# Optimization experiments

Hardware: AMD Instinct MI355X
Metric: run time of the kernel (lower is better)

Reference implementation:

```python
import jax, jax.numpy as jnp
import numpy as np

B, N, D = 32, 20, 64          # graph pairs, max node set size, node state dim
NODE_F, EDGE_F = 16, 8        # raw feature dims
E_PER, PROP = 40, 5           # edges per graph, propagation steps
NC2 = N * (N - 1) // 2        # 190
TEMP, ITERS = 0.1, 20         # sinkhorn temperature / iterations
SRC, DST = np.triu_indices(N, 1)   # source_list / destination_list (len NC2)


def _lin(k, fin, fout):
    return jax.random.normal(k, (fin, fout), dtype=jnp.float32) / np.sqrt(fin).astype(np.float32)


def setup_inputs():
    key = jax.random.key(0)
    ks = jax.random.split(key, 24)
    tn, te = 2 * B * N, 2 * B * E_PER
    gid = jnp.repeat(jnp.arange(2 * B), E_PER)   # edges stay within their graph
    inp = {
        'node_features': jax.random.normal(ks[0], (tn, NODE_F), jnp.float32),
        'edge_features': jax.random.normal(ks[1], (te, EDGE_F), jnp.float32),
        'query_adj': (jax.random.uniform(ks[2], (B, N, N)) < 0.3).astype(jnp.float32),
        'corpus_adj': (jax.random.uniform(ks[3], (B, N, N)) < 0.3).astype(jnp.float32),
        'from_idx': jax.random.randint(ks[4], (te,), 0, N) + gid * N,
        'to_idx': jax.random.randint(ks[5], (te,), 0, N) + gid * N,
    }
    # GraphEncoder
    inp['Wn'] = _lin(ks[6], NODE_F, D); inp['bn'] = jnp.zeros(D)
    inp['We'] = _lin(ks[7], EDGE_F, D); inp['be'] = jnp.zeros(D)
    # GraphPropLayer: message net (in 3D) and node-update net (in 2D)
    inp['Wm1'] = _lin(ks[8], 3 * D, D); inp['bm1'] = jnp.zeros(D)
    inp['Wm2'] = _lin(ks[9], D, D);     inp['bm2'] = jnp.zeros(D)
    inp['Wu1'] = _lin(ks[10], 2 * D, D); inp['bu1'] = jnp.zeros(D)
    inp['Wu2'] = _lin(ks[11], D, D);     inp['bu2'] = jnp.zeros(D)
    # node_sinkhorn_feature_layers: Linear(D,N) -> ReLU -> Linear(N,N)
    inp['Ws1'] = _lin(ks[12], D, N); inp['bs1'] = jnp.zeros(N)
    inp['Ws2'] = _lin(ks[13], N, N); inp['bs2'] = jnp.zeros(N)
    # lrl_network: Linear(2D+1, D) -> ReLU -> Linear(D, D)
    inp['Wl1'] = _lin(ks[14], 2 * D + 1, D); inp['bl1'] = jnp.zeros(D)
    inp['Wl2'] = _lin(ks[15], D, D);         inp['bl2'] = jnp.zeros(D)
    return inp


def _mlp2(x, W1, b1, W2, b2):
    return jax.nn.relu(x @ W1 + b1) @ W2 + b2


def _sinkhorn(log_alpha):
    la = log_alpha / TEMP
    for _ in range(ITERS):
        la = la - jax.nn.logsumexp(la, axis=2, keepdims=True)
        la = la - jax.nn.logsumexp(la, axis=1, keepdims=True)
    return jnp.exp(la)


def _nc2_edge_emb(H, adj, Wl1, bl1, Wl2, bl2):
    s, d = H[:, SRC], H[:, DST]          # [B, NC2, D]
    e = adj[:, SRC, DST][..., None]      # [B, NC2, 1]
    fwd = _mlp2(jnp.concatenate([s, d, e], -1), Wl1, bl1, Wl2, bl2)
    bwd = _mlp2(jnp.concatenate([d, s, e], -1), Wl1, bl1, Wl2, bl2)
    return fwd + bwd


def reference(node_features, edge_features, query_adj, corpus_adj, from_idx, to_idx,
              Wn, bn, We, be, Wm1, bm1, Wm2, bm2, Wu1, bu1, Wu2, bu2,
              Ws1, bs1, Ws2, bs2, Wl1, bl1, Wl2, bl2):
    # encoder
    h = node_features @ Wn + bn
    e = edge_features @ We + be
    # GMN-style gather -> MLP -> scatter propagation
    for _ in range(PROP):
        msg = _mlp2(jnp.concatenate([h[from_idx], h[to_idx], e], -1), Wm1, bm1, Wm2, bm2)
        agg = jax.ops.segment_sum(msg, to_idx, num_segments=2 * B * N)
        h = _mlp2(jnp.concatenate([h, agg], -1), Wu1, bu1, Wu2, bu2)
    # split_and_stack (all graphs have exactly N nodes): query even, corpus odd
    H = h.reshape(2 * B, N, D)
    Hq, Hc = H[0::2], H[1::2]
    # node Sinkhorn over L1 cdist of transformed features
    Tq = _mlp2(Hq, Ws1, bs1, Ws2, bs2)
    Tc = _mlp2(Hc, Ws1, bs1, Ws2, bs2)
    cost = jnp.abs(Tq[:, :, None, :] - Tc[:, None, :, :]).sum(-1)   # [B, N, N]
    P = _sinkhorn(-cost)                                            # node transport plan
    qe = _nc2_edge_emb(Hq, query_adj, Wl1, bl1, Wl2, bl2)           # [B, NC2, D]
    ce = _nc2_edge_emb(Hc, corpus_adj, Wl1, bl1, Wl2, bl2)
    # 4-way gather-multiply edge scores: [B, NC2, NC2]
    straight = P[:, SRC[:, None], SRC[None, :]] * P[:, DST[:, None], DST[None, :]]
    cross = P[:, SRC[:, None], DST[None, :]] * P[:, DST[:, None], SRC[None, :]]
    esi = jnp.maximum(straight, cross)                              # use_max=True
    eplan = _sinkhorn(jnp.log(esi + 1e-6))                          # use_second_sinkhorn_log
    # use_m_ms_edge=True: pairwise asymmetric L1 alignment distance
    diff = qe[:, :, None, :] - ce[:, None, :, :]                    # [B, NC2, NC2, D]
    dist = (eplan * (jax.nn.relu(diff).sum(-1) + jax.nn.relu(-diff).sum(-1))).sum((-1, -2))
    return dist                                                      # [B]
```

## Files before the change

### kernel.cpp

```cpp
#include <hip/hip_runtime.h>
#include <math.h>

#define B_     32
#define N_     20
#define D_     64
#define NODE_F 16
#define EDGE_F 8
#define E_PER  40
#define PROP   5
#define NC2    190
#define ITERS  20
#define INV_TEMP 10.0f
#define TN (2*B_*N_)
#define NG (2*B_)

struct PairTab { int s[NC2]; int d[NC2]; };
constexpr PairTab make_pairs() {
    PairTab t{};
    int idx = 0;
    for (int i = 0; i < N_; ++i)
        for (int j = i + 1; j < N_; ++j) { t.s[idx] = i; t.d[idx] = j; ++idx; }
    return t;
}
__device__ constexpr PairTab PAIRS = make_pairs();

__device__ __forceinline__ float rlane(float x, int k) {
    return __int_as_float(__builtin_amdgcn_readlane(__float_as_int(x), k));
}
template<int CTRL>
__device__ __forceinline__ float dppmov(float x) {
    return __int_as_float(__builtin_amdgcn_update_dpp(
        0, __float_as_int(x), CTRL, 0xf, 0xf, false));
}
__device__ __forceinline__ float rowsum16(float x) {
    x += dppmov<0x121>(x); x += dppmov<0x122>(x);
    x += dppmov<0x124>(x); x += dppmov<0x128>(x);
    return x;
}
__device__ __forceinline__ float rowmax16(float x) {
    x = fmaxf(x, dppmov<0x121>(x)); x = fmaxf(x, dppmov<0x122>(x));
    x = fmaxf(x, dppmov<0x124>(x)); x = fmaxf(x, dppmov<0x128>(x));
    return x;
}
__device__ __forceinline__ float nrcp(float x) {
    float r = __builtin_amdgcn_rcpf(x);
    r = r * fmaf(-x, r, 2.0f);
    return r;
}

__global__ __launch_bounds__(1024, 4) void k_prop(
    const float* __restrict__ nf, const float* __restrict__ ef,
    const int* __restrict__ fidx, const int* __restrict__ tidx,
    const float* __restrict__ Wn, const float* __restrict__ bn,
    const float* __restrict__ We, const float* __restrict__ be,
    const float* __restrict__ Wm1, const float* __restrict__ bm1,
    const float* __restrict__ Wm2, const float* __restrict__ bm2,
    const float* __restrict__ Wu1, const float* __restrict__ bu1,
    const float* __restrict__ Wu2, const float* __restrict__ bu2,
    float* __restrict__ hout)
{
    __shared__ __align__(16) float wbuf[8192];
    __shared__ float sh[20][64];
    __shared__ float sE1[40][64];
    __shared__ float sFT[40][64];
    __shared__ float sa[20][64];
    __shared__ short sF[40], sD[40];
    int g = blockIdx.x, t = threadIdx.x, w = t >> 6, l = t & 63;

    if (t < 40) {
        sF[t] = (short)(fidx[g * 40 + t] - g * 20);
        sD[t] = (short)(tidx[g * 40 + t] - g * 20);
    }
    for (int n = w; n < 20; n += 16) {
        float a = bn[l];
#pragma unroll
        for (int k = 0; k < NODE_F; ++k) a += nf[(g * 20 + n) * NODE_F + k] * Wn[k * 64 + l];
        sh[n][l] = a; sa[n][l] = 0.f;
    }
    {
        const float4* s4 = (const float4*)(Wm1 + 128 * 64);
        float4* d4 = (float4*)wbuf;
        for (int i = t; i < 1024; i += 1024) d4[i] = s4[i];
    }
    __syncthreads();
    for (int e = w; e < 40; e += 16) {
        float em = be[l];
#pragma unroll
        for (int k = 0; k < EDGE_F; ++k) em += ef[(g * 40 + e) * EDGE_F + k] * We[k * 64 + l];
        float a = bm1[l];
#pragma unroll 4
        for (int k = 0; k < 64; ++k) a += rlane(em, k) * wbuf[k * 64 + l];
        sE1[e][l] = a;
    }

    for (int step = 0; step < PROP; ++step) {
        __syncthreads();
        {
            const float4* s4 = (const float4*)Wm1;
            float4* d4 = (float4*)wbuf;
            for (int i = t; i < 2048; i += 1024) d4[i] = s4[i];
        }
        __syncthreads();
        {
            int part = w >> 3;
            int wl = w & 7;
            for (int n = wl; n < 20; n += 8) {
                float xh = sh[n][l];
                float a = 0.f;
#pragma unroll 4
                for (int k = 0; k < 64; ++k)
                    a += rlane(xh, k) * wbuf[(part * 64 + k) * 64 + l];
                sFT[part * 20 + n][l] = a;
            }
        }
        __syncthreads();
        {
            const float4* s4 = (const float4*)Wm2;
            float4* d4 = (float4*)wbuf;
            for (int i = t; i < 1024; i += 1024) d4[i] = s4[i];
        }
        __syncthreads();
        for (int e = w; e < 40; e += 16) {
            int fr = sF[e], to = sD[e];
            float a1 = fmaxf(sFT[fr][l] + sFT[20 + to][l] + sE1[e][l], 0.f);
            float o = bm2[l];
#pragma unroll 4
            for (int k = 0; k < 64; ++k) o += rlane(a1, k) * wbuf[k * 64 + l];
            atomicAdd(&sa[to][l], o);
        }
        __syncthreads();
        {
            const float4* s4 = (const float4*)Wu1;
            float4* d4 = (float4*)wbuf;
            for (int i = t; i < 2048; i += 1024) d4[i] = s4[i];
        }
        __syncthreads();
        float a2[2];
#pragma unroll
        for (int ii = 0; ii < 2; ++ii) {
            int n = w + 16 * ii;
            if (n < 20) {
                float xh = sh[n][l], xa = sa[n][l];
                float a = bu1[l];
#pragma unroll 4
                for (int k = 0; k < 64; ++k) {
                    a += rlane(xh, k) * wbuf[k * 64 + l];
                    a += rlane(xa, k) * wbuf[(64 + k) * 64 + l];
                }
                a2[ii] = fmaxf(a, 0.f);
            } else a2[ii] = 0.f;
        }
        __syncthreads();
        {
            const float4* s4 = (const float4*)Wu2;
            float4* d4 = (float4*)wbuf;
            for (int i = t; i < 1024; i += 1024) d4[i] = s4[i];
        }
        __syncthreads();
#pragma unroll
        for (int ii = 0; ii < 2; ++ii) {
            int n = w + 16 * ii;
            if (n < 20) {
                float o = bu2[l];
#pragma unroll 4
                for (int k = 0; k < 64; ++k) o += rlane(a2[ii], k) * wbuf[k * 64 + l];
                sh[n][l] = o; sa[n][l] = 0.f;
            }
        }
    }
    __syncthreads();
    for (int n = w; n < 20; n += 16) hout[(g * 20 + n) * 64 + l] = sh[n][l];
}

__global__ __launch_bounds__(1024, 4) void k_fuse(
    const float* __restrict__ h,
    const float* __restrict__ qadj, const float* __restrict__ cadj,
    const float* __restrict__ Ws1, const float* __restrict__ bs1,
    const float* __restrict__ Ws2, const float* __restrict__ bs2,
    const float* __restrict__ Wl1, const float* __restrict__ bl1,
    const float* __restrict__ Wl2, const float* __restrict__ bl2,
    float* __restrict__ emb, float* __restrict__ eplan, float* __restrict__ dout)
{
    __shared__ short sQs[192], sQd[192];
    __shared__ float sP[N_][N_];
    __shared__ float sVbuf[192];
    __shared__ __align__(16) float region[12800];
    int t = threadIdx.x, w = t >> 6, l = t & 63;

    if (t < 192) {
        int tt = t < NC2 ? t : NC2 - 1;
        sQs[t] = (short)PAIRS.s[tt]; sQd[t] = (short)PAIRS.d[tt];
    }
    __syncthreads();

    if (blockIdx.x < 32) {
        int b = blockIdx.x;
        if (t == 0) dout[b] = 0.f;
        float* sT = region;
        float* sLa = region + 800;

        {
            int lk = (l < 20) ? l : 0;
#pragma unroll
            for (int s = 0; s < 3; ++s) {
                int r = w + 16 * s;
                if (r < 40) {
                    float hv = h[(b * 40 + r) * 64 + l];
                    float a = bs1[lk];
#pragma unroll 4
                    for (int ff = 0; ff < 64; ++ff) a += rlane(hv, ff) * Ws1[ff * 20 + lk];
                    a = fmaxf(a, 0.f);
                    float t2 = bs2[lk];
#pragma unroll
                    for (int j = 0; j < 20; ++j) t2 += rlane(a, j) * Ws2[j * 20 + lk];
                    if (l < 20) sT[(r >= 20) * 400 + (r % 20) * 20 + l] = t2;
                }
            }
        }
        __syncthreads();
        if (t < 400) {
            int i = t / 20, j = t % 20;
            float c = 0.f;
#pragma unroll
            for (int k = 0; k < 20; ++k) c += fabsf(sT[i * 20 + k] - sT[400 + j * 20 + k]);
            sLa[i * 20 + j] = -c * INV_TEMP;
        }
        __syncthreads();

        if (w == 0) {
            int q = l & 31, r2 = l >> 5;
            bool qok = (q < 20);
            float A20[10], u10[10];
#pragma unroll
            for (int i = 0; i < 10; ++i) {
                int r = 2 * i + r2;
                A20[i] = qok ? sLa[r * 20 + q] : -1e30f;
            }
            float vq = 0.f;
            for (int it = 0; it < ITERS; ++it) {
#pragma unroll
                for (int i = 0; i < 10; ++i) {
                    float x = A20[i] - vq;
                    float m = x;
#pragma unroll
                    for (int off = 16; off; off >>= 1) m = fmaxf(m, __shfl_xor(m, off));
                    float s = __expf(x - m);
#pragma unroll
                    for (int off = 16; off; off >>= 1) s += __shfl_xor(s, off);
                    u10[i] = m + __logf(s);
                }
                float pm = -1e30f;
#pragma unroll
                for (int i = 0; i < 10; ++i) pm = fmaxf(pm, A20[i] - u10[i]);
                float ps = 0.f;
#pragma unroll
                for (int i = 0; i < 10; ++i) ps += __expf(A20[i] - u10[i] - pm);
                float om = __shfl_xor(pm, 32), os = __shfl_xor(ps, 32);
                float M = fmaxf(pm, om);
                float S = ps * __expf(pm - M) + os * __expf(om - M);
                vq = M + __logf(S);
                if (!qok) vq = 0.f;
            }
#pragma unroll
            for (int i = 0; i < 10; ++i) {
                int r = 2 * i + r2;
                if (qok) sP[r][q] = __expf(A20[i] - u10[i] - vq);
            }
        }
        __syncthreads();

        int g4 = l >> 4, l16 = l & 15, rslot = w * 4 + g4;
        int sp[3], dp[3]; bool pv[3];
#pragma unroll
        for (int i = 0; i < 3; ++i) {
            int p = rslot + 64 * i;
            pv[i] = (p < NC2);
            int pc = pv[i] ? p : 0;
            sp[i] = sQs[pc]; dp[i] = sQd[pc];
        }
        int sq[12], dq[12]; bool qv[12];
#pragma unroll
        for (int j = 0; j < 12; ++j) {
            int q = l16 + 16 * j;
            qv[j] = (q < NC2);
            int qc = qv[j] ? q : 0;
            sq[j] = sQs[qc]; dq[j] = sQd[qc];
        }

        float AE[3][12];
#pragma unroll
        for (int i = 0; i < 3; ++i)
#pragma unroll
            for (int j = 0; j < 12; ++j) {
                if (pv[i] && qv[j]) {
                    float st = sP[sp[i]][sq[j]] * sP[dp[i]][dq[j]];
                    float cr = sP[sp[i]][dq[j]] * sP[dp[i]][sq[j]];
                    AE[i][j] = __logf(fmaxf(st, cr) + 1e-6f) * INV_TEMP;
                } else AE[i][j] = -1e30f;
            }

        float u[3];
#pragma unroll
        for (int i = 0; i < 3; ++i) {
            float m = -1e30f;
#pragma unroll
            for (int j = 0; j < 12; ++j) m = fmaxf(m, AE[i][j]);
            m = rowmax16(m);
            float s = 0.f;
#pragma unroll
            for (int j = 0; j < 12; ++j) s += __expf(AE[i][j] - m);
            s = rowsum16(s);
            u[i] = m + __logf(s);
            if (!pv[i]) u[i] = 0.f;
        }
#pragma unroll
        for (int j = 0; j < 12; ++j) {
            float pm = -1e30f;
#pragma unroll
            for (int i = 0; i < 3; ++i) if (pv[i]) pm = fmaxf(pm, AE[i][j] - u[i]);
            pm = fmaxf(pm, __shfl_xor(pm, 16));
            pm = fmaxf(pm, __shfl_xor(pm, 32));
            if (g4 == 0) region[w * 200 + l16 + 16 * j] = pm;
        }
        __syncthreads();
        if (t < 192) {
            float M = -1e30f;
#pragma unroll
            for (int s = 0; s < 16; ++s) M = fmaxf(M, region[s * 200 + t]);
            sVbuf[t] = M;
        }
        __syncthreads();
        float Mj[12];
#pragma unroll
        for (int j = 0; j < 12; ++j) Mj[j] = sVbuf[l16 + 16 * j];
#pragma unroll
        for (int j = 0; j < 12; ++j) {
            float ps = 0.f;
#pragma unroll
            for (int i = 0; i < 3; ++i) if (pv[i]) ps += __expf(AE[i][j] - u[i] - Mj[j]);
            ps += __shfl_xor(ps, 16);
            ps += __shfl_xor(ps, 32);
            if (g4 == 0) region[w * 200 + l16 + 16 * j] = ps;
        }
        __syncthreads();
        if (t < 192) {
            float S = 0.f;
#pragma unroll
            for (int s = 0; s < 16; ++s) S += region[s * 200 + t];
            sVbuf[t] = sVbuf[t] + __logf(fmaxf(S, 1e-37f));
        }
        __syncthreads();
#pragma unroll
        for (int j = 0; j < 12; ++j) Mj[j] = sVbuf[l16 + 16 * j];
#pragma unroll
        for (int i = 0; i < 3; ++i)
#pragma unroll
            for (int j = 0; j < 12; ++j) {
                float e = __expf(AE[i][j] - u[i] - Mj[j]);
                AE[i][j] = (pv[i] && qv[j]) ? e : 0.f;
            }
        __syncthreads();

        float invS[3];
        for (int it = 0; it < ITERS - 1; ++it) {
#pragma unroll
            for (int i = 0; i < 3; ++i) {
                float s01 = AE[i][0] + AE[i][1], s23 = AE[i][2] + AE[i][3];
                float s45 = AE[i][4] + AE[i][5], s67 = AE[i][6] + AE[i][7];
                float s89 = AE[i][8] + AE[i][9], sab = AE[i][10] + AE[i][11];
                float S = ((s01 + s23) + (s45 + s67)) + (s89 + sab);
                S = rowsum16(S);
                invS[i] = nrcp(fmaxf(S, 1e-30f));
            }
#pragma unroll
            for (int j = 0; j < 12; ++j) {
                float pc = AE[0][j] * invS[0];
                pc = fmaf(AE[1][j], invS[1], pc);
                pc = fmaf(AE[2][j], invS[2], pc);
                pc += __shfl_xor(pc, 16);
                pc += __shfl_xor(pc, 32);
                if (g4 == 0) region[w * 200 + l16 + 16 * j] = pc;
            }
            __syncthreads();
            if (t < 192) {
                float c = 0.f;
#pragma unroll
                for (int s = 0; s < 16; ++s) c += region[s * 200 + t];
                sVbuf[t] = nrcp(fmaxf(c, 1e-30f));
            }
            __syncthreads();
            float ic[12];
#pragma unroll
            for (int j = 0; j < 12; ++j) ic[j] = sVbuf[l16 + 16 * j];
#pragma unroll
            for (int i = 0; i < 3; ++i)
#pragma unroll
                for (int j = 0; j < 12; ++j) {
                    float tmp = AE[i][j] * invS[i];
                    AE[i][j] = tmp * ic[j];
                }
        }

        float* ep = eplan + (size_t)b * NC2 * NC2;
#pragma unroll
        for (int i = 0; i < 3; ++i) {
            if (pv[i]) {
                int p = rslot + 64 * i;
                float* row = ep + (size_t)p * NC2;
#pragma unroll
                for (int j = 0; j < 12; ++j)
                    if (qv[j]) row[l16 + 16 * j] = AE[i][j];
            }
        }
    } else {
        int eb = blockIdx.x - 32, b = eb >> 2, qt = eb & 3;
        float* wb1 = region;
        float* wb2 = region + 8192;
        {
            const float4* s1 = (const float4*)Wl1;
            float4* d1 = (float4*)wb1;
            for (int i = t; i < 2048; i += 1024) d1[i] = s1[i];
            const float4* s2 = (const float4*)Wl2;
            float4* d2 = (float4*)wb2;
            if (t < 1024) d2[t] = s2[t];
        }
        float b1 = bl1[l];
        float w128 = Wl1[128 * 64 + l];
        float b2 = 2.f * bl2[l];
        __syncthreads();

        int base = qt * 96 + w * 6;
        float sv[6], dv[6], av[6]; bool val[6]; int gg[6], pp[6];
#pragma unroll
        for (int s = 0; s < 6; ++s) {
            int pl = base + s;
            val[s] = (pl < 380);
            int plc = val[s] ? pl : 0;
            gg[s] = (plc >= 190) ? 1 : 0;
            pp[s] = plc - gg[s] * 190;
            int sp = sQs[pp[s]], dp = sQd[pp[s]];
            sv[s] = h[(b * 40 + gg[s] * 20 + sp) * 64 + l];
            dv[s] = h[(b * 40 + gg[s] * 20 + dp) * 64 + l];
            const float* adj = gg[s] ? cadj : qadj;
            av[s] = adj[b * 400 + sp * 20 + dp];
        }
        float aF[6], aB[6];
#pragma unroll
        for (int s = 0; s < 6; ++s) { float t0 = b1 + av[s] * w128; aF[s] = t0; aB[s] = t0; }
#pragma unroll 2
        for (int k = 0; k < 64; ++k) {
            float w0 = wb1[k * 64 + l];
            float w1 = wb1[(64 + k) * 64 + l];
#pragma unroll
            for (int s = 0; s < 6; ++s) {
                float a = rlane(sv[s], k), c = rlane(dv[s], k);
                aF[s] += a * w0 + c * w1;
                aB[s] += c * w0 + a * w1;
            }
        }
        float hs[6], out[6];
#pragma unroll
        for (int s = 0; s < 6; ++s) { hs[s] = fmaxf(aF[s], 0.f) + fmaxf(aB[s], 0.f); out[s] = b2; }
#pragma unroll 4
        for (int k = 0; k < 64; ++k) {
            float ww = wb2[k * 64 + l];
#pragma unroll
            for (int s = 0; s < 6; ++s) out[s] += rlane(hs[s], k) * ww;
        }
#pragma unroll
        for (int s = 0; s < 6; ++s)
            if (val[s]) emb[((size_t)(2 * b + gg[s]) * NC2 + pp[s]) * 64 + l] = out[s];
    }
}

__global__ __launch_bounds__(256) void k_dist(
    const float* __restrict__ emb, const float* __restrict__ eplan, float* __restrict__ dout)
{
    int b = blockIdx.x, c = blockIdx.y;
    int w = threadIdx.x >> 6, l = threadIdx.x & 63;
    const float* qe = emb + (size_t)(2 * b) * NC2 * D_;
    const float* ce = emb + (size_t)(2 * b + 1) * NC2 * D_;
    const float* W = eplan + (size_t)b * NC2 * NC2;
    float acc = 0.f;
    int pbase = c * 16 + w * 4;
    for (int i = 0; i < 4; ++i) {
        int p = pbase + i;
        if (p >= NC2) break;
        float qv = qe[(size_t)p * D_ + l];
        const float* wrow = W + (size_t)p * NC2;
        for (int q = 0; q < NC2; ++q)
            acc += wrow[q] * fabsf(qv - ce[(size_t)q * D_ + l]);
    }
#pragma unroll
    for (int off = 32; off; off >>= 1) acc += __shfl_xor(acc, off);
    if (l == 0) atomicAdd(&dout[b], acc);
}

extern "C" void kernel_launch(void* const* d_in, const int* in_sizes, int n_in,
                              void* d_out, int out_size, void* d_ws, size_t ws_size,
                              hipStream_t stream)
{
    const float* nf   = (const float*)d_in[0];
    const float* ef   = (const float*)d_in[1];
    const float* qadj = (const float*)d_in[2];
    const float* cadj = (const float*)d_in[3];
    const int*   fidx = (const int*)d_in[4];
    const int*   tidx = (const int*)d_in[5];
    const float* Wn  = (const float*)d_in[6];  const float* bn  = (const float*)d_in[7];
    const float* We  = (const float*)d_in[8];  const float* be  = (const float*)d_in[9];
    const float* Wm1 = (const float*)d_in[10]; const float* bm1 = (const float*)d_in[11];
    const float* Wm2 = (const float*)d_in[12]; const float* bm2 = (const float*)d_in[13];
    const float* Wu1 = (const float*)d_in[14]; const float* bu1 = (const float*)d_in[15];
    const float* Wu2 = (const float*)d_in[16]; const float* bu2 = (const float*)d_in[17];
    const float* Ws1 = (const float*)d_in[18]; const float* bs1 = (const float*)d_in[19];
    const float* Ws2 = (const float*)d_in[20]; const float* bs2 = (const float*)d_in[21];
    const float* Wl1 = (const float*)d_in[22]; const float* bl1 = (const float*)d_in[23];
    const float* Wl2 = (const float*)d_in[24]; const float* bl2 = (const float*)d_in[25];

    float* ws    = (float*)d_ws;
    float* h     = ws;
    float* emb   = h + (size_t)TN * 64;
    float* eplan = emb + (size_t)NG * NC2 * 64;
    float* dout  = (float*)d_out;

    k_prop<<<NG, 1024, 0, stream>>>(nf, ef, fidx, tidx, Wn, bn, We, be,
                                    Wm1, bm1, Wm2, bm2, Wu1, bu1, Wu2, bu2, h);
    k_fuse<<<160, 1024, 0, stream>>>(h, qadj, cadj, Ws1, bs1, Ws2, bs2,
                                     Wl1, bl1, Wl2, bl2, emb, eplan, dout);
    k_dist<<<dim3(B_, 12), 256, 0, stream>>>(emb, eplan, dout);
}
```

Measured before the change: 350.9 us.

## Batch multiple rows per warp in propagation and halve fuse block size

In the propagation kernel, each warp now computes two or three node/edge rows in one pass over the shared weight buffer, so each weight load is reused across rows. The node update is split across two warp halves writing partial sums that are combined afterwards. The fuse kernel drops to 512 threads per block, with each thread holding twice as many sinkhorn rows in registers and a finer-grained edge-embedding grid of 254 blocks. The intent is better weight reuse and occupancy; the risk is register pressure from the larger per-thread arrays.

```diff
diff --git a/kernel.cpp b/kernel.cpp
--- a/kernel.cpp
+++ b/kernel.cpp
@@ -60,12 +60,13 @@
     float* __restrict__ hout)
 {
     __shared__ __align__(16) float wbuf[8192];
-    __shared__ float sh[20][64];
-    __shared__ float sE1[40][64];
-    __shared__ float sFT[40][64];
-    __shared__ float sa[20][64];
+    __shared__ __align__(16) float sh[20][64];
+    __shared__ __align__(16) float sE1[40][64];
+    __shared__ __align__(16) float sFT[40][64];
+    __shared__ __align__(16) float sa[20][64];
     __shared__ short sF[40], sD[40];
     int g = blockIdx.x, t = threadIdx.x, w = t >> 6, l = t & 63;
+    int part = w >> 3, wl = w & 7;
 
     if (t < 40) {
         sF[t] = (short)(fidx[g * 40 + t] - g * 20);
@@ -80,17 +81,31 @@
     {
         const float4* s4 = (const float4*)(Wm1 + 128 * 64);
         float4* d4 = (float4*)wbuf;
-        for (int i = t; i < 1024; i += 1024) d4[i] = s4[i];
+        if (t < 1024) d4[t] = s4[t];
     }
     __syncthreads();
-    for (int e = w; e < 40; e += 16) {
-        float em = be[l];
-#pragma unroll
-        for (int k = 0; k < EDGE_F; ++k) em += ef[(g * 40 + e) * EDGE_F + k] * We[k * 64 + l];
-        float a = bm1[l];
-#pragma unroll 4
-        for (int k = 0; k < 64; ++k) a += rlane(em, k) * wbuf[k * 64 + l];
-        sE1[e][l] = a;
+    {
+        int e0 = w, e1 = w + 16, e2 = w + 32;
+        bool h2 = (w < 8);
+        int e2c = h2 ? e2 : 0;
+        float m0 = be[l], m1 = be[l], m2 = be[l];
+#pragma unroll
+        for (int k = 0; k < EDGE_F; ++k) {
+            float wv = We[k * 64 + l];
+            m0 += ef[(g * 40 + e0) * EDGE_F + k] * wv;
+            m1 += ef[(g * 40 + e1) * EDGE_F + k] * wv;
+            m2 += ef[(g * 40 + e2c) * EDGE_F + k] * wv;
+        }
+        float a0 = bm1[l], a1 = a0, a2 = a0;
+#pragma unroll 4
+        for (int k = 0; k < 64; ++k) {
+            float wv = wbuf[k * 64 + l];
+            a0 += rlane(m0, k) * wv;
+            a1 += rlane(m1, k) * wv;
+            a2 += rlane(m2, k) * wv;
+        }
+        sE1[e0][l] = a0; sE1[e1][l] = a1;
+        if (h2) sE1[e2][l] = a2;
     }
 
     for (int step = 0; step < PROP; ++step) {
@@ -98,81 +113,105 @@
         {
             const float4* s4 = (const float4*)Wm1;
             float4* d4 = (float4*)wbuf;
-            for (int i = t; i < 2048; i += 1024) d4[i] = s4[i];
-        }
-        __syncthreads();
-        {
-            int part = w >> 3;
-            int wl = w & 7;
-            for (int n = wl; n < 20; n += 8) {
-                float xh = sh[n][l];
-                float a = 0.f;
-#pragma unroll 4
-                for (int k = 0; k < 64; ++k)
-                    a += rlane(xh, k) * wbuf[(part * 64 + k) * 64 + l];
-                sFT[part * 20 + n][l] = a;
-            }
+            d4[t] = s4[t]; d4[t + 1024] = s4[t + 1024];
+        }
+        __syncthreads();
+        {
+            bool h2 = (wl < 4);
+            float x0 = sh[wl][l], x1 = sh[wl + 8][l];
+            float x2 = h2 ? sh[wl + 16][l] : 0.f;
+            float a0 = 0.f, a1 = 0.f, a2 = 0.f;
+#pragma unroll 4
+            for (int k = 0; k < 64; ++k) {
+                float wv = wbuf[(part * 64 + k) * 64 + l];
+                a0 += rlane(x0, k) * wv;
+                a1 += rlane(x1, k) * wv;
+                a2 += rlane(x2, k) * wv;
+            }
+            sFT[part * 20 + wl][l] = a0;
+            sFT[part * 20 + wl + 8][l] = a1;
+            if (h2) sFT[part * 20 + wl + 16][l] = a2;
         }
         __syncthreads();
         {
             const float4* s4 = (const float4*)Wm2;
             float4* d4 = (float4*)wbuf;
-            for (int i = t; i < 1024; i += 1024) d4[i] = s4[i];
-        }
-        __syncthreads();
-        for (int e = w; e < 40; e += 16) {
-            int fr = sF[e], to = sD[e];
-            float a1 = fmaxf(sFT[fr][l] + sFT[20 + to][l] + sE1[e][l], 0.f);
-            float o = bm2[l];
-#pragma unroll 4
-            for (int k = 0; k < 64; ++k) o += rlane(a1, k) * wbuf[k * 64 + l];
-            atomicAdd(&sa[to][l], o);
+            if (t < 1024) d4[t] = s4[t];
+        }
+        __syncthreads();
+        {
+            bool h2 = (w < 8);
+            int e0 = w, e1 = w + 16, e2c = h2 ? w + 32 : 0;
+            int f0 = sF[e0], d0 = sD[e0];
+            int f1 = sF[e1], d1 = sD[e1];
+            int f2 = sF[e2c], d2 = sD[e2c];
+            float p0 = fmaxf(sFT[f0][l] + sFT[20 + d0][l] + sE1[e0][l], 0.f);
+            float p1 = fmaxf(sFT[f1][l] + sFT[20 + d1][l] + sE1[e1][l], 0.f);
+            float p2 = fmaxf(sFT[f2][l] + sFT[20 + d2][l] + sE1[e2c][l], 0.f);
+            float o0 = bm2[l], o1 = o0, o2 = o0;
+#pragma unroll 4
+            for (int k = 0; k < 64; ++k) {
+                float wv = wbuf[k * 64 + l];
+                o0 += rlane(p0, k) * wv;
+                o1 += rlane(p1, k) * wv;
+                o2 += rlane(p2, k) * wv;
+            }
+            atomicAdd(&sa[d0][l], o0);
+            atomicAdd(&sa[d1][l], o1);
+            if (h2) atomicAdd(&sa[d2][l], o2);
         }
         __syncthreads();
         {
             const float4* s4 = (const float4*)Wu1;
             float4* d4 = (float4*)wbuf;
-            for (int i = t; i < 2048; i += 1024) d4[i] = s4[i];
-        }
-        __syncthreads();
-        float a2[2];
-#pragma unroll
-        for (int ii = 0; ii < 2; ++ii) {
-            int n = w + 16 * ii;
-            if (n < 20) {
-                float xh = sh[n][l], xa = sa[n][l];
-                float a = bu1[l];
-#pragma unroll 4
-                for (int k = 0; k < 64; ++k) {
-                    a += rlane(xh, k) * wbuf[k * 64 + l];
-                    a += rlane(xa, k) * wbuf[(64 + k) * 64 + l];
-                }
-                a2[ii] = fmaxf(a, 0.f);
-            } else a2[ii] = 0.f;
+            d4[t] = s4[t]; d4[t + 1024] = s4[t + 1024];
+        }
+        __syncthreads();
+        {
+            bool h2 = (wl < 4);
+            float y0 = part ? sa[wl][l] : sh[wl][l];
+            float y1 = part ? sa[wl + 8][l] : sh[wl + 8][l];
+            float y2 = h2 ? (part ? sa[wl + 16][l] : sh[wl + 16][l]) : 0.f;
+            float a0 = 0.f, a1 = 0.f, a2 = 0.f;
+#pragma unroll 4
+            for (int k = 0; k < 64; ++k) {
+                float wv = wbuf[(part * 64 + k) * 64 + l];
+                a0 += rlane(y0, k) * wv;
+                a1 += rlane(y1, k) * wv;
+                a2 += rlane(y2, k) * wv;
+            }
+            sFT[part * 20 + wl][l] = a0;
+            sFT[part * 20 + wl + 8][l] = a1;
+            if (h2) sFT[part * 20 + wl + 16][l] = a2;
         }
         __syncthreads();
         {
             const float4* s4 = (const float4*)Wu2;
             float4* d4 = (float4*)wbuf;
-            for (int i = t; i < 1024; i += 1024) d4[i] = s4[i];
-        }
-        __syncthreads();
-#pragma unroll
-        for (int ii = 0; ii < 2; ++ii) {
-            int n = w + 16 * ii;
-            if (n < 20) {
-                float o = bu2[l];
-#pragma unroll 4
-                for (int k = 0; k < 64; ++k) o += rlane(a2[ii], k) * wbuf[k * 64 + l];
-                sh[n][l] = o; sa[n][l] = 0.f;
-            }
+            if (t < 1024) d4[t] = s4[t];
+        }
+        __syncthreads();
+        {
+            bool h1 = (w < 4);
+            int n0 = w, n1c = h1 ? w + 16 : 0;
+            float z0 = fmaxf(sFT[n0][l] + sFT[20 + n0][l] + bu1[l], 0.f);
+            float z1 = fmaxf(sFT[n1c][l] + sFT[20 + n1c][l] + bu1[l], 0.f);
+            float o0 = bu2[l], o1 = o0;
+#pragma unroll 4
+            for (int k = 0; k < 64; ++k) {
+                float wv = wbuf[k * 64 + l];
+                o0 += rlane(z0, k) * wv;
+                o1 += rlane(z1, k) * wv;
+            }
+            sh[n0][l] = o0; sa[n0][l] = 0.f;
+            if (h1) { sh[n1c][l] = o1; sa[n1c][l] = 0.f; }
         }
     }
     __syncthreads();
     for (int n = w; n < 20; n += 16) hout[(g * 20 + n) * 64 + l] = sh[n][l];
 }
 
-__global__ __launch_bounds__(1024, 4) void k_fuse(
+__global__ __launch_bounds__(512, 2) void k_fuse(
     const float* __restrict__ h,
     const float* __restrict__ qadj, const float* __restrict__ cadj,
     const float* __restrict__ Ws1, const float* __restrict__ bs1,
@@ -184,7 +223,7 @@
     __shared__ short sQs[192], sQd[192];
     __shared__ float sP[N_][N_];
     __shared__ float sVbuf[192];
-    __shared__ __align__(16) float region[12800];
+    __shared__ __align__(16) float region[12288];
     int t = threadIdx.x, w = t >> 6, l = t & 63;
 
     if (t < 192) {
@@ -196,25 +235,24 @@
     if (blockIdx.x < 32) {
         int b = blockIdx.x;
         if (t == 0) dout[b] = 0.f;
-        float* sT = region;
-        float* sLa = region + 800;
+        float* colpart = region;
+        float* sT = region + 1600;
+        float* sLa = region + 2400;
 
         {
             int lk = (l < 20) ? l : 0;
 #pragma unroll
-            for (int s = 0; s < 3; ++s) {
-                int r = w + 16 * s;
-                if (r < 40) {
-                    float hv = h[(b * 40 + r) * 64 + l];
-                    float a = bs1[lk];
-#pragma unroll 4
-                    for (int ff = 0; ff < 64; ++ff) a += rlane(hv, ff) * Ws1[ff * 20 + lk];
-                    a = fmaxf(a, 0.f);
-                    float t2 = bs2[lk];
-#pragma unroll
-                    for (int j = 0; j < 20; ++j) t2 += rlane(a, j) * Ws2[j * 20 + lk];
-                    if (l < 20) sT[(r >= 20) * 400 + (r % 20) * 20 + l] = t2;
-                }
+            for (int s = 0; s < 5; ++s) {
+                int r = w + 8 * s;
+                float hv = h[(b * 40 + r) * 64 + l];
+                float a = bs1[lk];
+#pragma unroll 4
+                for (int ff = 0; ff < 64; ++ff) a += rlane(hv, ff) * Ws1[ff * 20 + lk];
+                a = fmaxf(a, 0.f);
+                float t2 = bs2[lk];
+#pragma unroll
+                for (int j = 0; j < 20; ++j) t2 += rlane(a, j) * Ws2[j * 20 + lk];
+                if (l < 20) sT[(r >= 20) * 400 + (r % 20) * 20 + l] = t2;
             }
         }
         __syncthreads();
@@ -270,10 +308,10 @@
         __syncthreads();
 
         int g4 = l >> 4, l16 = l & 15, rslot = w * 4 + g4;
-        int sp[3], dp[3]; bool pv[3];
-#pragma unroll
-        for (int i = 0; i < 3; ++i) {
-            int p = rslot + 64 * i;
+        int sp[6], dp[6]; bool pv[6];
+#pragma unroll
+        for (int i = 0; i < 6; ++i) {
+            int p = rslot + 32 * i;
             pv[i] = (p < NC2);
             int pc = pv[i] ? p : 0;
             sp[i] = sQs[pc]; dp[i] = sQd[pc];
@@ -287,9 +325,9 @@
             sq[j] = sQs[qc]; dq[j] = sQd[qc];
         }
 
-        float AE[3][12];
-#pragma unroll
-        for (int i = 0; i < 3; ++i)
+        float AE[6][12];
+#pragma unroll
+        for (int i = 0; i < 6; ++i)
 #pragma unroll
             for (int j = 0; j < 12; ++j) {
                 if (pv[i] && qv[j]) {
@@ -299,9 +337,9 @@
                 } else AE[i][j] = -1e30f;
             }
 
-        float u[3];
-#pragma unroll
-        for (int i = 0; i < 3; ++i) {
+        float u[6];
+#pragma unroll
+        for (int i = 0; i < 6; ++i) {
             float m = -1e30f;
 #pragma unroll
             for (int j = 0; j < 12; ++j) m = fmaxf(m, AE[i][j]);
@@ -317,16 +355,16 @@
         for (int j = 0; j < 12; ++j) {
             float pm = -1e30f;
 #pragma unroll
-            for (int i = 0; i < 3; ++i) if (pv[i]) pm = fmaxf(pm, AE[i][j] - u[i]);
+            for (int i = 0; i < 6; ++i) if (pv[i]) pm = fmaxf(pm, AE[i][j] - u[i]);
             pm = fmaxf(pm, __shfl_xor(pm, 16));
             pm = fmaxf(pm, __shfl_xor(pm, 32));
-            if (g4 == 0) region[w * 200 + l16 + 16 * j] = pm;
+            if (g4 == 0) colpart[w * 200 + l16 + 16 * j] = pm;
         }
         __syncthreads();
         if (t < 192) {
             float M = -1e30f;
 #pragma unroll
-            for (int s = 0; s < 16; ++s) M = fmaxf(M, region[s * 200 + t]);
+            for (int s = 0; s < 8; ++s) M = fmaxf(M, colpart[s * 200 + t]);
             sVbuf[t] = M;
         }
         __syncthreads();
@@ -337,23 +375,23 @@
         for (int j = 0; j < 12; ++j) {
             float ps = 0.f;
 #pragma unroll
-            for (int i = 0; i < 3; ++i) if (pv[i]) ps += __expf(AE[i][j] - u[i] - Mj[j]);
+            for (int i = 0; i < 6; ++i) if (pv[i]) ps += __expf(AE[i][j] - u[i] - Mj[j]);
             ps += __shfl_xor(ps, 16);
             ps += __shfl_xor(ps, 32);
-            if (g4 == 0) region[w * 200 + l16 + 16 * j] = ps;
+            if (g4 == 0) colpart[w * 200 + l16 + 16 * j] = ps;
         }
         __syncthreads();
         if (t < 192) {
             float S = 0.f;
 #pragma unroll
-            for (int s = 0; s < 16; ++s) S += region[s * 200 + t];
+            for (int s = 0; s < 8; ++s) S += colpart[s * 200 + t];
             sVbuf[t] = sVbuf[t] + __logf(fmaxf(S, 1e-37f));
         }
         __syncthreads();
 #pragma unroll
         for (int j = 0; j < 12; ++j) Mj[j] = sVbuf[l16 + 16 * j];
 #pragma unroll
-        for (int i = 0; i < 3; ++i)
+        for (int i = 0; i < 6; ++i)
 #pragma unroll
             for (int j = 0; j < 12; ++j) {
                 float e = __expf(AE[i][j] - u[i] - Mj[j]);
@@ -361,10 +399,10 @@
             }
         __syncthreads();
 
-        float invS[3];
+        float invS[6];
         for (int it = 0; it < ITERS - 1; ++it) {
 #pragma unroll
-            for (int i = 0; i < 3; ++i) {
+            for (int i = 0; i < 6; ++i) {
                 float s01 = AE[i][0] + AE[i][1], s23 = AE[i][2] + AE[i][3];
                 float s45 = AE[i][4] + AE[i][5], s67 = AE[i][6] + AE[i][7];
                 float s89 = AE[i][8] + AE[i][9], sab = AE[i][10] + AE[i][11];
@@ -377,15 +415,18 @@
                 float pc = AE[0][j] * invS[0];
                 pc = fmaf(AE[1][j], invS[1], pc);
                 pc = fmaf(AE[2][j], invS[2], pc);
+                pc = fmaf(AE[3][j], invS[3], pc);
+                pc = fmaf(AE[4][j], invS[4], pc);
+                pc = fmaf(AE[5][j], invS[5], pc);
                 pc += __shfl_xor(pc, 16);
                 pc += __shfl_xor(pc, 32);
-                if (g4 == 0) region[w * 200 + l16 + 16 * j] = pc;
+                if (g4 == 0) colpart[w * 200 + l16 + 16 * j] = pc;
             }
             __syncthreads();
             if (t < 192) {
                 float c = 0.f;
 #pragma unroll
-                for (int s = 0; s < 16; ++s) c += region[s * 200 + t];
+                for (int s = 0; s < 8; ++s) c += colpart[s * 200 + t];
                 sVbuf[t] = nrcp(fmaxf(c, 1e-30f));
             }
             __syncthreads();
@@ -393,7 +434,7 @@
 #pragma unroll
             for (int j = 0; j < 12; ++j) ic[j] = sVbuf[l16 + 16 * j];
 #pragma unroll
-            for (int i = 0; i < 3; ++i)
+            for (int i = 0; i < 6; ++i)
 #pragma unroll
                 for (int j = 0; j < 12; ++j) {
                     float tmp = AE[i][j] * invS[i];
@@ -403,9 +444,9 @@
 
         float* ep = eplan + (size_t)b * NC2 * NC2;
 #pragma unroll
-        for (int i = 0; i < 3; ++i) {
+        for (int i = 0; i < 6; ++i) {
             if (pv[i]) {
-                int p = rslot + 64 * i;
+                int p = rslot + 32 * i;
                 float* row = ep + (size_t)p * NC2;
 #pragma unroll
                 for (int j = 0; j < 12; ++j)
@@ -413,36 +454,39 @@
             }
         }
     } else {
-        int eb = blockIdx.x - 32, b = eb >> 2, qt = eb & 3;
+        int eb = blockIdx.x - 32;
         float* wb1 = region;
         float* wb2 = region + 8192;
         {
             const float4* s1 = (const float4*)Wl1;
             float4* d1 = (float4*)wb1;
-            for (int i = t; i < 2048; i += 1024) d1[i] = s1[i];
+#pragma unroll
+            for (int i = 0; i < 4; ++i) d1[t + 512 * i] = s1[t + 512 * i];
             const float4* s2 = (const float4*)Wl2;
             float4* d2 = (float4*)wb2;
-            if (t < 1024) d2[t] = s2[t];
+#pragma unroll
+            for (int i = 0; i < 2; ++i) d2[t + 512 * i] = s2[t + 512 * i];
         }
         float b1 = bl1[l];
         float w128 = Wl1[128 * 64 + l];
         float b2 = 2.f * bl2[l];
         __syncthreads();
 
-        int base = qt * 96 + w * 6;
-        float sv[6], dv[6], av[6]; bool val[6]; int gg[6], pp[6];
+        int base = eb * 48 + w * 6;
+        float sv[6], dv[6], av[6]; bool val[6]; int gi[6], pp[6];
 #pragma unroll
         for (int s = 0; s < 6; ++s) {
-            int pl = base + s;
-            val[s] = (pl < 380);
-            int plc = val[s] ? pl : 0;
-            gg[s] = (plc >= 190) ? 1 : 0;
-            pp[s] = plc - gg[s] * 190;
-            int sp = sQs[pp[s]], dp = sQd[pp[s]];
-            sv[s] = h[(b * 40 + gg[s] * 20 + sp) * 64 + l];
-            dv[s] = h[(b * 40 + gg[s] * 20 + dp) * 64 + l];
-            const float* adj = gg[s] ? cadj : qadj;
-            av[s] = adj[b * 400 + sp * 20 + dp];
+            int sid = base + s;
+            val[s] = (sid < NG * NC2);
+            int sc = val[s] ? sid : 0;
+            gi[s] = sc / NC2;
+            pp[s] = sc - gi[s] * NC2;
+            int bb = gi[s] >> 1, gg = gi[s] & 1;
+            int spi = sQs[pp[s]], dpi = sQd[pp[s]];
+            sv[s] = h[(bb * 40 + gg * 20 + spi) * 64 + l];
+            dv[s] = h[(bb * 40 + gg * 20 + dpi) * 64 + l];
+            const float* adj = gg ? cadj : qadj;
+            av[s] = adj[bb * 400 + spi * 20 + dpi];
         }
         float aF[6], aB[6];
 #pragma unroll
@@ -469,7 +513,7 @@
         }
 #pragma unroll
         for (int s = 0; s < 6; ++s)
-            if (val[s]) emb[((size_t)(2 * b + gg[s]) * NC2 + pp[s]) * 64 + l] = out[s];
+            if (val[s]) emb[((size_t)gi[s] * NC2 + pp[s]) * 64 + l] = out[s];
     }
 }
 
@@ -525,7 +569,7 @@
 
     k_prop<<<NG, 1024, 0, stream>>>(nf, ef, fidx, tidx, Wn, bn, We, be,
                                     Wm1, bm1, Wm2, bm2, Wu1, bu1, Wu2, bu2, h);
-    k_fuse<<<160, 1024, 0, stream>>>(h, qadj, cadj, Ws1, bs1, Ws2, bs2,
-                                     Wl1, bl1, Wl2, bl2, emb, eplan, dout);
+    k_fuse<<<32 + 254, 512, 0, stream>>>(h, qadj, cadj, Ws1, bs1, Ws2, bs2,
+                                         Wl1, bl1, Wl2, bl2, emb, eplan, dout);
     k_dist<<<dim3(B_, 12), 256, 0, stream>>>(emb, eplan, dout);
 }
```

Result: no change. 357.7 us (+1.9%).
